# Performance work log

Hardware: AMD Instinct MI355X
Metric: run time of the kernel (lower is better)

The kernel has to match this reference:

```python
import jax, jax.numpy as jnp
import numpy as np

N_NODES = 100000
N_EDGES = 1600000
D_IN, D_HID, D_OUT = 128, 256, 128


def _sage_conv(x, src, dst, W_l, b_l, W_r, num_nodes):
    """PyG SAGEConv with mean aggregation: lin_l(mean_j x_j) + lin_r(x_i)."""
    msg = x[src]                                              # [E, d] gather
    agg = jax.ops.segment_sum(msg, dst, num_segments=num_nodes)   # [N, d]
    cnt = jax.ops.segment_sum(jnp.ones((src.shape[0],), x.dtype), dst,
                              num_segments=num_nodes)         # [N]
    agg = agg / jnp.maximum(cnt, 1.0)[:, None]                # mean (0 for isolated)
    return agg @ W_l + b_l + x @ W_r


def setup_inputs() -> dict:
    key = jax.random.key(0)
    ks = jax.random.split(key, 8)
    x = jax.random.normal(ks[0], (N_NODES, D_IN), dtype=jnp.float32)
    edge_index = jax.random.randint(ks[1], (2, N_EDGES), 0, N_NODES, dtype=jnp.int64)
    perturb_first = jax.random.normal(ks[2], (N_NODES, D_HID), dtype=jnp.float32) * 0.05
    perturb_last = jax.random.normal(ks[3], (N_NODES, D_OUT), dtype=jnp.float32) * 0.05
    s1 = 1.0 / np.sqrt(D_IN)
    s2 = 1.0 / np.sqrt(D_HID)
    return {
        "x": x,
        "edge_index": edge_index,
        "perturb_first": perturb_first,
        "perturb_last": perturb_last,
        "Wl1": jax.random.normal(ks[4], (D_IN, D_HID), dtype=jnp.float32) * s1,
        "bl1": jnp.zeros((D_HID,), dtype=jnp.float32),
        "Wr1": jax.random.normal(ks[5], (D_IN, D_HID), dtype=jnp.float32) * s1,
        "Wl2": jax.random.normal(ks[6], (D_HID, D_OUT), dtype=jnp.float32) * s2,
        "bl2": jnp.zeros((D_OUT,), dtype=jnp.float32),
        "Wr2": jax.random.normal(ks[7], (D_HID, D_OUT), dtype=jnp.float32) * s2,
    }


def reference(x, edge_index, perturb_first, perturb_last,
              Wl1, bl1, Wr1, Wl2, bl2, Wr2):
    # PyG default flow source_to_target: messages from edge_index[0] -> edge_index[1]
    src, dst = edge_index[0], edge_index[1]
    n = x.shape[0]
    # forward() only applies model[0] and model[3] (the two SAGEConvs);
    # the LayerNorm/PReLU entries in the Sequential are skipped.
    h = _sage_conv(x, src, dst, Wl1, bl1, Wr1, n) + perturb_first
    out = _sage_conv(h, src, dst, Wl2, bl2, Wr2, n) + perturb_last
    return out
```

## Files before the change

### kernel.cpp

```cpp
#include <hip/hip_runtime.h>

#define N_NODES 100000
#define N_EDGES 1600000
#define NBUCK 196
#define CAP_BIN 64
#define CAP_B 12288

typedef float v4f __attribute__((ext_vector_type(4)));
typedef __bf16 v8bf __attribute__((ext_vector_type(8)));
typedef __bf16 v4bf __attribute__((ext_vector_type(4)));
typedef unsigned int v4u __attribute__((ext_vector_type(4)));

union FragU { v4u u; v8bf b; };
union PkU { unsigned int u; __bf16 h[2]; };
union Pk2 { uint2 u2; __bf16 h[4]; };

__device__ __forceinline__ int clampN(int v) {
    return v < 0 ? 0 : (v >= N_NODES ? N_NODES - 1 : v);
}
__device__ __forceinline__ float bfhi(unsigned int u) { return __uint_as_float(u & 0xffff0000u); }
__device__ __forceinline__ float bflo(unsigned int u) { return __uint_as_float(u << 16); }

__global__ __launch_bounds__(256) void k_count(
    const int* __restrict__ dst, int* __restrict__ bucketCnt)
{
    __shared__ int h[NBUCK];
    const int tid = threadIdx.x;
    for (int i = tid; i < NBUCK; i += 256) h[i] = 0;
    __syncthreads();
    int e0 = blockIdx.x * 4096;
    int e1 = e0 + 4096; if (e1 > N_EDGES) e1 = N_EDGES;
    for (int e = e0 + tid; e < e1; e += 256)
        atomicAdd(&h[clampN(dst[e]) >> 9], 1);
    __syncthreads();
    for (int i = tid; i < NBUCK; i += 256)
        if (h[i]) atomicAdd(&bucketCnt[i], h[i]);
}

__global__ __launch_bounds__(256) void k_scanb(
    const int* __restrict__ bucketCnt, int* __restrict__ baseB,
    int* __restrict__ gcur, int* __restrict__ rowp)
{
    const int t = threadIdx.x;
    int v = (t < NBUCK) ? bucketCnt[t] : 0;
    int incl = v;
    #pragma unroll
    for (int off = 1; off < 64; off <<= 1) {
        int u = __shfl_up(incl, off);
        if ((t & 63) >= off) incl += u;
    }
    __shared__ int wt[4];
    if ((t & 63) == 63) wt[t >> 6] = incl;
    __syncthreads();
    int woff = 0;
    #pragma unroll
    for (int k = 0; k < 4; ++k) if (k < (t >> 6)) woff += wt[k];
    int excl = woff + incl - v;
    if (t < NBUCK) { baseB[t] = excl; gcur[t] = excl; }
    if (t == NBUCK) { baseB[NBUCK] = excl; rowp[N_NODES] = excl; }
}

__global__ __launch_bounds__(256) void k_bin(
    const int* __restrict__ src, const int* __restrict__ dst,
    int* __restrict__ gcur, unsigned int* __restrict__ packed)
{
    __shared__ unsigned int bins[256 * CAP_BIN];
    __shared__ int cnt[256];
    const int tid = threadIdx.x;
    cnt[tid] = 0;
    __syncthreads();
    const int epb = (N_EDGES + gridDim.x - 1) / gridDim.x;
    int e0 = blockIdx.x * epb;
    int e1 = e0 + epb; if (e1 > N_EDGES) e1 = N_EDGES;
    for (int ch = e0; ch < e1; ch += 4096) {
        int chEnd = ch + 4096; if (chEnd > e1) chEnd = e1;
        for (int e = ch + tid; e < chEnd; e += 256) {
            int s = clampN(src[e]);
            int d = clampN(dst[e]);
            unsigned int val = (unsigned int)s | ((unsigned int)(d & 511) << 17);
            int b = d >> 9;
            int slot = atomicAdd(&cnt[b], 1);
            if (slot < CAP_BIN) bins[b * CAP_BIN + slot] = val;
            else {
                int g = atomicAdd(&gcur[b], 1);
                packed[g] = val;
            }
        }
        __syncthreads();
        int n = cnt[tid]; if (n > CAP_BIN) n = CAP_BIN;
        if (tid < NBUCK && n > 0) {
            int g = atomicAdd(&gcur[tid], n);
            for (int j = 0; j < n; ++j) packed[g + j] = bins[tid * CAP_BIN + j];
        }
        __syncthreads();
        cnt[tid] = 0;
        __syncthreads();
    }
}

__global__ __launch_bounds__(256) void k_bucket(
    const int* __restrict__ baseB, const unsigned int* __restrict__ packed,
    int* __restrict__ rowp, int* __restrict__ edge_src)
{
    __shared__ int hist[512], cur[512];
    __shared__ int wt[4];
    __shared__ unsigned int buf[CAP_B];
    const int b = blockIdx.x, tid = threadIdx.x;
    const int lo = baseB[b], hi = baseB[b + 1], c = hi - lo;
    for (int i = tid; i < 512; i += 256) hist[i] = 0;
    __syncthreads();
    for (int e = tid; e < c; e += 256)
        atomicAdd(&hist[packed[lo + e] >> 17], 1);
    __syncthreads();
    int a0 = hist[2 * tid], a1 = hist[2 * tid + 1];
    int s = a0 + a1;
    int incl = s;
    #pragma unroll
    for (int off = 1; off < 64; off <<= 1) {
        int u = __shfl_up(incl, off);
        if ((tid & 63) >= off) incl += u;
    }
    if ((tid & 63) == 63) wt[tid >> 6] = incl;
    __syncthreads();
    int woff = 0;
    #pragma unroll
    for (int k = 0; k < 4; ++k) if (k < (tid >> 6)) woff += wt[k];
    int ep = woff + incl - s;
    cur[2 * tid] = ep;
    cur[2 * tid + 1] = ep + a0;
    int n0 = b * 512 + 2 * tid;
    if (n0 < N_NODES)     rowp[n0]     = lo + ep;
    if (n0 + 1 < N_NODES) rowp[n0 + 1] = lo + ep + a0;
    __syncthreads();
    for (int e = tid; e < c; e += 256) {
        unsigned int v = packed[lo + e];
        int dl = v >> 17;
        unsigned int sv = v & 0x1FFFFu;
        int pos = atomicAdd(&cur[dl], 1);
        if (pos < CAP_B) buf[pos] = sv;
        else edge_src[lo + pos] = (int)sv;
    }
    __syncthreads();
    int cc = c < CAP_B ? c : CAP_B;
    for (int e = tid; e < cc; e += 256) edge_src[lo + e] = (int)buf[e];
}

__global__ __launch_bounds__(256) void k_cvt_x(
    const float* __restrict__ x, __bf16* __restrict__ a2, int n4)
{
    int t = blockIdx.x * 256 + threadIdx.x;
    if (t >= n4) return;
    float4 v = ((const float4*)x)[t];
    int row = t >> 5, c4 = t & 31;
    v4bf o = { (__bf16)v.x, (__bf16)v.y, (__bf16)v.z, (__bf16)v.w };
    *(v4bf*)(a2 + (size_t)row * 256 + 128 + c4 * 4) = o;
}

__global__ __launch_bounds__(256) void k_pack_w(
    const float* __restrict__ W, __bf16* __restrict__ Wp, int K, int N)
{
    int t = blockIdx.x * 256 + threadIdx.x;
    int NT = N >> 4;
    int total = (K >> 5) * NT * 64;
    if (t >= total) return;
    int l = t & 63;
    int fi = t >> 6;
    int kc = fi / NT, nt = fi % NT;
    int k0 = kc * 32 + (l >> 4) * 8;
    int col = nt * 16 + (l & 15);
    v8bf o;
    #pragma unroll
    for (int j = 0; j < 8; ++j) o[j] = (__bf16)W[(size_t)(k0 + j) * N + col];
    *(v8bf*)(Wp + (size_t)t * 8) = o;
}

template<int MODE>
__global__ __launch_bounds__(256) void k_gather16(
    const int* __restrict__ rp, const int* __restrict__ es,
    const __bf16* __restrict__ tab, void* __restrict__ outp)
{
    int wid = (blockIdx.x * 256 + threadIdx.x) >> 6;
    int l = threadIdx.x & 63;
    if (wid >= N_NODES) return;
    int start = rp[wid], end = rp[wid + 1];
    const int slot = l >> 4, c = l & 15;
    float s0 = 0.f, s1 = 0.f, s2 = 0.f, s3 = 0.f;
    float s4 = 0.f, s5 = 0.f, s6 = 0.f, s7 = 0.f;

    int e0 = start + slot;
    bool h0 = e0 < end;
    v4u r0 = {0, 0, 0, 0};
    if (h0) {
        int i0 = es[e0];
        r0 = (MODE == 0)
           ? *(const v4u*)(tab + (size_t)i0 * 256 + 128 + c * 8)
           : *(const v4u*)(tab + (size_t)i0 * 128 + c * 8);
    }
    int e1 = e0 + 4;
    bool h1 = e1 < end;
    int i1 = h1 ? es[e1] : 0;

    while (h0) {
        v4u r1 = {0, 0, 0, 0};
        if (h1) r1 = (MODE == 0)
                   ? *(const v4u*)(tab + (size_t)i1 * 256 + 128 + c * 8)
                   : *(const v4u*)(tab + (size_t)i1 * 128 + c * 8);
        int e2 = e1 + 4;
        bool h2 = e2 < end;
        int i2 = h2 ? es[e2] : 0;
        s0 += bflo(r0.x); s1 += bfhi(r0.x);
        s2 += bflo(r0.y); s3 += bfhi(r0.y);
        s4 += bflo(r0.z); s5 += bfhi(r0.z);
        s6 += bflo(r0.w); s7 += bfhi(r0.w);
        r0 = r1; h0 = h1; h1 = h2; i1 = i2; e1 = e2;
    }

    s0 += __shfl_xor(s0, 16); s1 += __shfl_xor(s1, 16);
    s2 += __shfl_xor(s2, 16); s3 += __shfl_xor(s3, 16);
    s4 += __shfl_xor(s4, 16); s5 += __shfl_xor(s5, 16);
    s6 += __shfl_xor(s6, 16); s7 += __shfl_xor(s7, 16);
    s0 += __shfl_xor(s0, 32); s1 += __shfl_xor(s1, 32);
    s2 += __shfl_xor(s2, 32); s3 += __shfl_xor(s3, 32);
    s4 += __shfl_xor(s4, 32); s5 += __shfl_xor(s5, 32);
    s6 += __shfl_xor(s6, 32); s7 += __shfl_xor(s7, 32);
    float invd = 1.f / fmaxf((float)(end - start), 1.f);
    if (slot == 0) {
        if (MODE == 0) {
            PkU a, b, cc, d;
            a.h[0] = (__bf16)(s0 * invd); a.h[1] = (__bf16)(s1 * invd);
            b.h[0] = (__bf16)(s2 * invd); b.h[1] = (__bf16)(s3 * invd);
            cc.h[0] = (__bf16)(s4 * invd); cc.h[1] = (__bf16)(s5 * invd);
            d.h[0] = (__bf16)(s6 * invd); d.h[1] = (__bf16)(s7 * invd);
            v4u o = { a.u, b.u, cc.u, d.u };
            ((v4u*)outp)[(size_t)wid * 32 + c] = o;
        } else {
            float4* o4 = (float4*)outp + (size_t)wid * 32 + c * 2;
            float4 va = o4[0], vb = o4[1];
            va.x += s0 * invd; va.y += s1 * invd; va.z += s2 * invd; va.w += s3 * invd;
            vb.x += s4 * invd; vb.y += s5 * invd; vb.z += s6 * invd; vb.w += s7 * invd;
            o4[0] = va; o4[1] = vb;
        }
    }
}

__device__ __forceinline__ void ld_stage(
    const __bf16* __restrict__ A, int tile, int tid, v4u st[4])
{
    const int row0 = tile * 64;
    #pragma unroll
    for (int cc = 0; cc < 4; ++cc) {
        int chunk = cc * 512 + tid;
        int row = chunk >> 5, col16 = chunk & 31;
        st[cc] = *(const v4u*)(A + (size_t)(row0 + row) * 256 + col16 * 8);
    }
}

template<int LAYER>
__global__ __launch_bounds__(512, 2) void k_gws(
    const __bf16* __restrict__ A,
    const __bf16* __restrict__ WpA, const __bf16* __restrict__ WpB,
    const float* __restrict__ bias, const float* __restrict__ pert,
    __bf16* __restrict__ outb, float* __restrict__ outf, int ntiles)
{
    __shared__ char aS[32768];
    __shared__ char hS[32768];
    const int tid = threadIdx.x;
    const int w = tid >> 6, l = tid & 63;
    const int lrow = l & 15, kg = l >> 4;
    const v4f zf = {0.f, 0.f, 0.f, 0.f};

    FragU bw[8][2];
    #pragma unroll
    for (int kc = 0; kc < 8; ++kc)
        #pragma unroll
        for (int nt = 0; nt < 2; ++nt) {
            const __bf16* Wp;
            int fi;
            if (LAYER == 1) {
                Wp = (kc < 4) ? WpA : WpB;
                fi = (kc & 3) * 16 + w * 2 + nt;
            } else {
                Wp = (w < 4) ? WpA : WpB;
                fi = kc * 8 + (w & 3) * 2 + nt;
            }
            bw[kc][nt].u = *(const v4u*)(Wp + ((size_t)fi * 64 + l) * 8);
        }

    int tile = blockIdx.x;
    v4u st[4];
    if (tile < ntiles) ld_stage(A, tile, tid, st);

    for (; tile < ntiles; tile += gridDim.x) {
        #pragma unroll
        for (int cc = 0; cc < 4; ++cc) {
            int chunk = cc * 512 + tid;
            int row = chunk >> 5, col16 = chunk & 31;
            int byte = (row * 512 + col16 * 16) ^ ((row & 7) << 4);
            *(v4u*)(aS + byte) = st[cc];
        }
        int nxt = tile + (int)gridDim.x;
        if (nxt < ntiles) ld_stage(A, nxt, tid, st);
        __syncthreads();

        const int row0 = tile * 64;
        #pragma unroll
        for (int rf = 0; rf < 4; ++rf) {
            const int arow = rf * 16 + lrow;
            FragU a[8];
            #pragma unroll
            for (int kc = 0; kc < 8; ++kc) {
                int byte = arow * 512 + ((kc * 64 + kg * 16) ^ ((arow & 7) << 4));
                a[kc].u = *(const v4u*)(aS + byte);
            }
            v4f acc[2] = {zf, zf};
            #pragma unroll
            for (int kc = 0; kc < 8; ++kc) {
                acc[0] = __builtin_amdgcn_mfma_f32_16x16x32_bf16(a[kc].b, bw[kc][0].b, acc[0], 0, 0, 0);
                acc[1] = __builtin_amdgcn_mfma_f32_16x16x32_bf16(a[kc].b, bw[kc][1].b, acc[1], 0, 0, 0);
            }
            #pragma unroll
            for (int nt = 0; nt < 2; ++nt)
                #pragma unroll
                for (int r = 0; r < 4; ++r) {
                    int row = rf * 16 + kg * 4 + r;
                    int col = w * 32 + nt * 16 + lrow;
                    int byte = (row * 512 + col * 2) ^ ((row & 7) << 4);
                    *(__bf16*)(hS + byte) = (__bf16)acc[nt][r];
                }
        }
        __syncthreads();

        #pragma unroll
        for (int it = 0; it < 8; ++it) {
            int chunk = it * 512 + tid;
            int row = chunk >> 6, c4 = chunk & 63;
            int grow = row0 + row;
            if (grow >= N_NODES) continue;
            int byte = (row * 512 + c4 * 8) ^ ((row & 7) << 4);
            Pk2 pk; pk.u2 = *(const uint2*)(hS + byte);
            if (LAYER == 1) {
                float4 pv = ((const float4*)pert)[(size_t)grow * 64 + c4];
                float4 bv = ((const float4*)bias)[c4];
                PkU o0, o1;
                o0.h[0] = (__bf16)((float)pk.h[0] + pv.x + bv.x);
                o0.h[1] = (__bf16)((float)pk.h[1] + pv.y + bv.y);
                o1.h[0] = (__bf16)((float)pk.h[2] + pv.z + bv.z);
                o1.h[1] = (__bf16)((float)pk.h[3] + pv.w + bv.w);
                uint2 ov = { o0.u, o1.u };
                *(uint2*)(outb + (size_t)grow * 256 + c4 * 4) = ov;
            } else {
                if (c4 < 32) {
                    *(uint2*)(outb + (size_t)grow * 128 + c4 * 4) = pk.u2;
                } else {
                    int oc4 = c4 - 32;
                    float4 pv = ((const float4*)pert)[(size_t)grow * 32 + oc4];
                    float4 bv = ((const float4*)bias)[oc4];
                    float4 ov;
                    ov.x = (float)pk.h[0] + pv.x + bv.x;
                    ov.y = (float)pk.h[1] + pv.y + bv.y;
                    ov.z = (float)pk.h[2] + pv.z + bv.z;
                    ov.w = (float)pk.h[3] + pv.w + bv.w;
                    ((float4*)outf)[(size_t)grow * 32 + oc4] = ov;
                }
            }
        }
    }
}

extern "C" void kernel_launch(void* const* d_in, const int* in_sizes, int n_in,
                              void* d_out, int out_size, void* d_ws, size_t ws_size,
                              hipStream_t stream)
{
    const float* x   = (const float*)d_in[0];
    const int*   ei  = (const int*)d_in[1];
    const float* p1  = (const float*)d_in[2];
    const float* p2  = (const float*)d_in[3];
    const float* Wl1 = (const float*)d_in[4];
    const float* bl1 = (const float*)d_in[5];
    const float* Wr1 = (const float*)d_in[6];
    const float* Wl2 = (const float*)d_in[7];
    const float* bl2 = (const float*)d_in[8];
    const float* Wr2 = (const float*)d_in[9];
    const int* src = ei;
    const int* dst = ei + N_EDGES;

    const size_t NPAD = (size_t)N_NODES + 64;
    char* wp = (char*)d_ws;
    __bf16* a2   = (__bf16*)wp; wp += NPAD * 256 * 2;
    __bf16* hb   = (__bf16*)wp; wp += NPAD * 256 * 2;
    __bf16* t2b  = (__bf16*)wp; wp += (size_t)N_NODES * 128 * 2;
    __bf16* Wl1p = (__bf16*)wp; wp += 128 * 256 * 2;
    __bf16* Wr1p = (__bf16*)wp; wp += 128 * 256 * 2;
    __bf16* Wl2p = (__bf16*)wp; wp += 256 * 128 * 2;
    __bf16* Wr2p = (__bf16*)wp; wp += 256 * 128 * 2;
    int* bucketCnt = (int*)wp; wp += 512 * 4;
    int* baseB     = (int*)wp; wp += 512 * 4;
    int* gcur      = (int*)wp; wp += 512 * 4;
    int* rowp      = (int*)wp; wp += (size_t)(N_NODES + 1) * 4 + 12;
    unsigned int* packed = (unsigned int*)wp; wp += (size_t)N_EDGES * 4;
    int* es        = (int*)wp;

    hipMemsetAsync(bucketCnt, 0, 512 * 4, stream);

    const int gblocks = (N_NODES * 64 + 255) / 256;
    const int n4 = N_NODES * 128 / 4;
    const int tiles = (N_NODES + 63) / 64;

    k_cvt_x<<<(n4 + 255) / 256, 256, 0, stream>>>(x, a2, n4);
    k_pack_w<<<16, 256, 0, stream>>>(Wl1, Wl1p, 128, 256);
    k_pack_w<<<16, 256, 0, stream>>>(Wr1, Wr1p, 128, 256);
    k_pack_w<<<16, 256, 0, stream>>>(Wl2, Wl2p, 256, 128);
    k_pack_w<<<16, 256, 0, stream>>>(Wr2, Wr2p, 256, 128);

    k_count<<<(N_EDGES + 4095) / 4096, 256, 0, stream>>>(dst, bucketCnt);
    k_scanb<<<1, 256, 0, stream>>>(bucketCnt, baseB, gcur, rowp);
    k_bin<<<256, 256, 0, stream>>>(src, dst, gcur, packed);
    k_bucket<<<NBUCK, 256, 0, stream>>>(baseB, packed, rowp, es);

    k_gather16<0><<<gblocks, 256, 0, stream>>>(rowp, es, a2, a2);
    k_gws<1><<<512, 512, 0, stream>>>(a2, Wl1p, Wr1p, bl1, p1, hb, nullptr, tiles);
    k_gws<2><<<512, 512, 0, stream>>>(hb, Wl2p, Wr2p, bl2, p2, t2b, (float*)d_out, tiles);
    k_gather16<1><<<gblocks, 256, 0, stream>>>(rowp, es, t2b, (void*)d_out);
}
```

Measured before the change: 340.1 us.

## Fuse prep kernels, deepen gather prefetch, write layer-2 epilogue to bf16 interleaved buffer

Merges the x conversion, four weight-packing launches and the edge bucket count into one k_prep launch to cut launch overhead. The layer-2 GEMM now writes both the transformed-neighbor half and the root+bias+perturb half as bf16 into one 256-wide buffer, and the final gather reads the root half from there instead of doing a read-modify-write on the fp32 output. The gather loop also prefetches two rows ahead instead of one. The cost is bf16 rounding of the root term and a larger workspace buffer.

```diff
diff --git a/kernel.cpp b/kernel.cpp
--- a/kernel.cpp
+++ b/kernel.cpp
@@ -5,6 +5,7 @@
 #define NBUCK 196
 #define CAP_BIN 64
 #define CAP_B 12288
+#define CVT_BLKS 12500
 
 typedef float v4f __attribute__((ext_vector_type(4)));
 typedef __bf16 v8bf __attribute__((ext_vector_type(8)));
@@ -21,20 +22,51 @@
 __device__ __forceinline__ float bfhi(unsigned int u) { return __uint_as_float(u & 0xffff0000u); }
 __device__ __forceinline__ float bflo(unsigned int u) { return __uint_as_float(u << 16); }
 
-__global__ __launch_bounds__(256) void k_count(
+__global__ __launch_bounds__(256) void k_prep(
+    const float* __restrict__ x, __bf16* __restrict__ a2,
+    const float* __restrict__ Wl1, const float* __restrict__ Wr1,
+    const float* __restrict__ Wl2, const float* __restrict__ Wr2,
+    __bf16* __restrict__ Wl1p, __bf16* __restrict__ Wr1p,
+    __bf16* __restrict__ Wl2p, __bf16* __restrict__ Wr2p,
     const int* __restrict__ dst, int* __restrict__ bucketCnt)
 {
-    __shared__ int h[NBUCK];
-    const int tid = threadIdx.x;
-    for (int i = tid; i < NBUCK; i += 256) h[i] = 0;
-    __syncthreads();
-    int e0 = blockIdx.x * 4096;
-    int e1 = e0 + 4096; if (e1 > N_EDGES) e1 = N_EDGES;
-    for (int e = e0 + tid; e < e1; e += 256)
-        atomicAdd(&h[clampN(dst[e]) >> 9], 1);
-    __syncthreads();
-    for (int i = tid; i < NBUCK; i += 256)
-        if (h[i]) atomicAdd(&bucketCnt[i], h[i]);
+    const int b = blockIdx.x, tid = threadIdx.x;
+    if (b < CVT_BLKS) {
+        int t = b * 256 + tid;
+        float4 v = ((const float4*)x)[t];
+        int row = t >> 5, c4 = t & 31;
+        v4bf o = { (__bf16)v.x, (__bf16)v.y, (__bf16)v.z, (__bf16)v.w };
+        *(v4bf*)(a2 + (size_t)row * 256 + 128 + c4 * 4) = o;
+    } else if (b < CVT_BLKS + 64) {
+        int pb = b - CVT_BLKS;
+        int which = pb >> 4;
+        int t = (pb & 15) * 256 + tid;
+        const float* W = which == 0 ? Wl1 : which == 1 ? Wr1 : which == 2 ? Wl2 : Wr2;
+        __bf16* Wp     = which == 0 ? Wl1p : which == 1 ? Wr1p : which == 2 ? Wl2p : Wr2p;
+        const int N = (which < 2) ? 256 : 128;
+        const int NT = N >> 4;
+        int l = t & 63;
+        int fi = t >> 6;
+        int kc = fi / NT, nt = fi % NT;
+        int k0 = kc * 32 + (l >> 4) * 8;
+        int col = nt * 16 + (l & 15);
+        v8bf o;
+        #pragma unroll
+        for (int j = 0; j < 8; ++j) o[j] = (__bf16)W[(size_t)(k0 + j) * N + col];
+        *(v8bf*)(Wp + (size_t)t * 8) = o;
+    } else {
+        __shared__ int h[NBUCK];
+        for (int i = tid; i < NBUCK; i += 256) h[i] = 0;
+        __syncthreads();
+        int cb = b - CVT_BLKS - 64;
+        int e0 = cb * 4096;
+        int e1 = e0 + 4096; if (e1 > N_EDGES) e1 = N_EDGES;
+        for (int e = e0 + tid; e < e1; e += 256)
+            atomicAdd(&h[clampN(dst[e]) >> 9], 1);
+        __syncthreads();
+        for (int i = tid; i < NBUCK; i += 256)
+            if (h[i]) atomicAdd(&bucketCnt[i], h[i]);
+    }
 }
 
 __global__ __launch_bounds__(256) void k_scanb(
@@ -145,35 +177,6 @@
     for (int e = tid; e < cc; e += 256) edge_src[lo + e] = (int)buf[e];
 }
 
-__global__ __launch_bounds__(256) void k_cvt_x(
-    const float* __restrict__ x, __bf16* __restrict__ a2, int n4)
-{
-    int t = blockIdx.x * 256 + threadIdx.x;
-    if (t >= n4) return;
-    float4 v = ((const float4*)x)[t];
-    int row = t >> 5, c4 = t & 31;
-    v4bf o = { (__bf16)v.x, (__bf16)v.y, (__bf16)v.z, (__bf16)v.w };
-    *(v4bf*)(a2 + (size_t)row * 256 + 128 + c4 * 4) = o;
-}
-
-__global__ __launch_bounds__(256) void k_pack_w(
-    const float* __restrict__ W, __bf16* __restrict__ Wp, int K, int N)
-{
-    int t = blockIdx.x * 256 + threadIdx.x;
-    int NT = N >> 4;
-    int total = (K >> 5) * NT * 64;
-    if (t >= total) return;
-    int l = t & 63;
-    int fi = t >> 6;
-    int kc = fi / NT, nt = fi % NT;
-    int k0 = kc * 32 + (l >> 4) * 8;
-    int col = nt * 16 + (l & 15);
-    v8bf o;
-    #pragma unroll
-    for (int j = 0; j < 8; ++j) o[j] = (__bf16)W[(size_t)(k0 + j) * N + col];
-    *(v8bf*)(Wp + (size_t)t * 8) = o;
-}
-
 template<int MODE>
 __global__ __launch_bounds__(256) void k_gather16(
     const int* __restrict__ rp, const int* __restrict__ es,
@@ -184,35 +187,32 @@
     if (wid >= N_NODES) return;
     int start = rp[wid], end = rp[wid + 1];
     const int slot = l >> 4, c = l & 15;
+    const size_t coff = (MODE == 0) ? (size_t)(128 + c * 8) : (size_t)(c * 8);
     float s0 = 0.f, s1 = 0.f, s2 = 0.f, s3 = 0.f;
     float s4 = 0.f, s5 = 0.f, s6 = 0.f, s7 = 0.f;
 
     int e0 = start + slot;
-    bool h0 = e0 < end;
-    v4u r0 = {0, 0, 0, 0};
-    if (h0) {
-        int i0 = es[e0];
-        r0 = (MODE == 0)
-           ? *(const v4u*)(tab + (size_t)i0 * 256 + 128 + c * 8)
-           : *(const v4u*)(tab + (size_t)i0 * 128 + c * 8);
-    }
     int e1 = e0 + 4;
-    bool h1 = e1 < end;
-    int i1 = h1 ? es[e1] : 0;
+    int e2 = e1 + 4;
+    bool h0 = e0 < end, h1 = e1 < end, h2 = e2 < end;
+    v4u r0 = {0, 0, 0, 0}, r1 = {0, 0, 0, 0};
+    if (h0) r0 = *(const v4u*)(tab + (size_t)es[e0] * 256 + coff);
+    if (h1) r1 = *(const v4u*)(tab + (size_t)es[e1] * 256 + coff);
+    int i2 = h2 ? es[e2] : 0;
 
     while (h0) {
-        v4u r1 = {0, 0, 0, 0};
-        if (h1) r1 = (MODE == 0)
-                   ? *(const v4u*)(tab + (size_t)i1 * 256 + 128 + c * 8)
-                   : *(const v4u*)(tab + (size_t)i1 * 128 + c * 8);
-        int e2 = e1 + 4;
-        bool h2 = e2 < end;
-        int i2 = h2 ? es[e2] : 0;
+        v4u r2 = {0, 0, 0, 0};
+        if (h2) r2 = *(const v4u*)(tab + (size_t)i2 * 256 + coff);
+        int e3 = e2 + 4;
+        bool h3 = e3 < end;
+        int i3 = h3 ? es[e3] : 0;
         s0 += bflo(r0.x); s1 += bfhi(r0.x);
         s2 += bflo(r0.y); s3 += bfhi(r0.y);
         s4 += bflo(r0.z); s5 += bfhi(r0.z);
         s6 += bflo(r0.w); s7 += bfhi(r0.w);
-        r0 = r1; h0 = h1; h1 = h2; i1 = i2; e1 = e2;
+        r0 = r1; r1 = r2;
+        h0 = h1; h1 = h2; h2 = h3;
+        i2 = i3; e2 = e3;
     }
 
     s0 += __shfl_xor(s0, 16); s1 += __shfl_xor(s1, 16);
@@ -234,11 +234,14 @@
             v4u o = { a.u, b.u, cc.u, d.u };
             ((v4u*)outp)[(size_t)wid * 32 + c] = o;
         } else {
-            float4* o4 = (float4*)outp + (size_t)wid * 32 + c * 2;
-            float4 va = o4[0], vb = o4[1];
-            va.x += s0 * invd; va.y += s1 * invd; va.z += s2 * invd; va.w += s3 * invd;
-            vb.x += s4 * invd; vb.y += s5 * invd; vb.z += s6 * invd; vb.w += s7 * invd;
-            o4[0] = va; o4[1] = vb;
+            v4u pu = *(const v4u*)(tab + (size_t)wid * 256 + 128 + c * 8);
+            float4 va, vb;
+            va.x = s0 * invd + bflo(pu.x); va.y = s1 * invd + bfhi(pu.x);
+            va.z = s2 * invd + bflo(pu.y); va.w = s3 * invd + bfhi(pu.y);
+            vb.x = s4 * invd + bflo(pu.z); vb.y = s5 * invd + bfhi(pu.z);
+            vb.z = s6 * invd + bflo(pu.w); vb.w = s7 * invd + bfhi(pu.w);
+            ((float4*)outp)[(size_t)wid * 32 + c * 2]     = va;
+            ((float4*)outp)[(size_t)wid * 32 + c * 2 + 1] = vb;
         }
     }
 }
@@ -260,7 +263,7 @@
     const __bf16* __restrict__ A,
     const __bf16* __restrict__ WpA, const __bf16* __restrict__ WpB,
     const float* __restrict__ bias, const float* __restrict__ pert,
-    __bf16* __restrict__ outb, float* __restrict__ outf, int ntiles)
+    __bf16* __restrict__ outb, int ntiles)
 {
     __shared__ char aS[32768];
     __shared__ char hS[32768];
@@ -349,19 +352,21 @@
                 uint2 ov = { o0.u, o1.u };
                 *(uint2*)(outb + (size_t)grow * 256 + c4 * 4) = ov;
             } else {
+                uint2 ov;
                 if (c4 < 32) {
-                    *(uint2*)(outb + (size_t)grow * 128 + c4 * 4) = pk.u2;
+                    ov = pk.u2;
                 } else {
                     int oc4 = c4 - 32;
                     float4 pv = ((const float4*)pert)[(size_t)grow * 32 + oc4];
                     float4 bv = ((const float4*)bias)[oc4];
-                    float4 ov;
-                    ov.x = (float)pk.h[0] + pv.x + bv.x;
-                    ov.y = (float)pk.h[1] + pv.y + bv.y;
-                    ov.z = (float)pk.h[2] + pv.z + bv.z;
-                    ov.w = (float)pk.h[3] + pv.w + bv.w;
-                    ((float4*)outf)[(size_t)grow * 32 + oc4] = ov;
+                    PkU o0, o1;
+                    o0.h[0] = (__bf16)((float)pk.h[0] + pv.x + bv.x);
+                    o0.h[1] = (__bf16)((float)pk.h[1] + pv.y + bv.y);
+                    o1.h[0] = (__bf16)((float)pk.h[2] + pv.z + bv.z);
+                    o1.h[1] = (__bf16)((float)pk.h[3] + pv.w + bv.w);
+                    ov.x = o0.u; ov.y = o1.u;
                 }
+                *(uint2*)(outb + (size_t)grow * 256 + c4 * 4) = ov;
             }
         }
     }
@@ -388,7 +393,7 @@
     char* wp = (char*)d_ws;
     __bf16* a2   = (__bf16*)wp; wp += NPAD * 256 * 2;
     __bf16* hb   = (__bf16*)wp; wp += NPAD * 256 * 2;
-    __bf16* t2b  = (__bf16*)wp; wp += (size_t)N_NODES * 128 * 2;
+    __bf16* u2b  = (__bf16*)wp; wp += NPAD * 256 * 2;
     __bf16* Wl1p = (__bf16*)wp; wp += 128 * 256 * 2;
     __bf16* Wr1p = (__bf16*)wp; wp += 128 * 256 * 2;
     __bf16* Wl2p = (__bf16*)wp; wp += 256 * 128 * 2;
@@ -403,22 +408,17 @@
     hipMemsetAsync(bucketCnt, 0, 512 * 4, stream);
 
     const int gblocks = (N_NODES * 64 + 255) / 256;
-    const int n4 = N_NODES * 128 / 4;
     const int tiles = (N_NODES + 63) / 64;
-
-    k_cvt_x<<<(n4 + 255) / 256, 256, 0, stream>>>(x, a2, n4);
-    k_pack_w<<<16, 256, 0, stream>>>(Wl1, Wl1p, 128, 256);
-    k_pack_w<<<16, 256, 0, stream>>>(Wr1, Wr1p, 128, 256);
-    k_pack_w<<<16, 256, 0, stream>>>(Wl2, Wl2p, 256, 128);
-    k_pack_w<<<16, 256, 0, stream>>>(Wr2, Wr2p, 256, 128);
-
-    k_count<<<(N_EDGES + 4095) / 4096, 256, 0, stream>>>(dst, bucketCnt);
+    const int prep_blocks = CVT_BLKS + 64 + (N_EDGES + 4095) / 4096;
+
+    k_prep<<<prep_blocks, 256, 0, stream>>>(
+        x, a2, Wl1, Wr1, Wl2, Wr2, Wl1p, Wr1p, Wl2p, Wr2p, dst, bucketCnt);
     k_scanb<<<1, 256, 0, stream>>>(bucketCnt, baseB, gcur, rowp);
     k_bin<<<256, 256, 0, stream>>>(src, dst, gcur, packed);
     k_bucket<<<NBUCK, 256, 0, stream>>>(baseB, packed, rowp, es);
 
     k_gather16<0><<<gblocks, 256, 0, stream>>>(rowp, es, a2, a2);
-    k_gws<1><<<512, 512, 0, stream>>>(a2, Wl1p, Wr1p, bl1, p1, hb, nullptr, tiles);
-    k_gws<2><<<512, 512, 0, stream>>>(hb, Wl2p, Wr2p, bl2, p2, t2b, (float*)d_out, tiles);
-    k_gather16<1><<<gblocks, 256, 0, stream>>>(rowp, es, t2b, (void*)d_out);
-}
+    k_gws<1><<<512, 512, 0, stream>>>(a2, Wl1p, Wr1p, bl1, p1, hb, tiles);
+    k_gws<2><<<512, 512, 0, stream>>>(hb, Wl2p, Wr2p, bl2, p2, u2b, tiles);
+    k_gather16<1><<<gblocks, 256, 0, stream>>>(rowp, es, u2b, (void*)d_out);
+}
```

Measured after the change: 317.4 us. -6.7%, faster.
